# Performance work log

Hardware: AMD Instinct MI355X
Metric: run time of the kernel (lower is better)

## Reference

```python
import jax, jax.numpy as jnp
import numpy as np

SEQ_LEN = 4096
N_FEAT = 2048
N_PADD = 128


def setup_inputs() -> dict:
    key = jax.random.key(0)
    kx, kw = jax.random.split(key)
    x = jax.random.normal(kx, (SEQ_LEN, N_FEAT), dtype=jnp.float32)
    # Fused QKV dense: features = 3 * n_feat
    W = jax.random.normal(kw, (N_FEAT, 3 * N_FEAT), dtype=jnp.float32) * (1.0 / np.sqrt(N_FEAT))
    b = jnp.zeros((3 * N_FEAT,), dtype=jnp.float32)
    return {"x": x, "W": W, "b": b, "n_padd": N_PADD}


def reference(x, W, b, n_padd):
    # Fused QKV projection, split along feature axis (as in nn.Dense + jnp.split)
    qkv = x @ W + b  # [S, 3F]
    q, k, v = jnp.split(qkv, 3, axis=1)  # each [S, F]
    S, F = q.shape
    idx = jnp.arange(S)
    # scores[i, j] = q_i . k_j / sqrt(F)
    scores = (q @ k.T) * (1.0 / jnp.sqrt(jnp.float32(F)))  # [S, S]
    seq_mask = idx >= n_padd                      # valid (non-padding) positions
    causal = idx[None, :] <= idx[:, None]         # j <= i
    mask = causal & seq_mask[None, :]             # kernel: causal_mask & seq_mask
    row_valid = seq_mask                          # rows < n_padd are not computed/stored
    neg_inf = jnp.float32(-jnp.inf)
    scores = jnp.where(mask, scores, neg_inf)
    # Fully-masked (padding) rows would softmax to NaN; neutralize then zero output.
    scores = jnp.where(row_valid[:, None], scores, 0.0)
    att = jax.nn.softmax(scores, axis=-1)         # row-wise stable softmax
    out = att @ v                                 # [S, F]
    out = jnp.where(row_valid[:, None], out, 0.0)  # padded rows produce zeros
    return out
```

## Files before the change

### kernel.cpp

```cpp
#include <hip/hip_runtime.h>
#include <cstdint>
#include <cstddef>
#include <cmath>

typedef unsigned short u16;
typedef short v8s __attribute__((ext_vector_type(8)));
typedef float v4f __attribute__((ext_vector_type(4)));

constexpr int SEQ = 4096;
constexpr int FEAT = 2048;
constexpr int F3 = 6144;


__device__ __forceinline__ u16 f2bf(float f) {
  union { float f; uint32_t u; } v; v.f = f;
  uint32_t r = v.u + 0x7FFFu + ((v.u >> 16) & 1u);
  return (u16)(r >> 16);
}

__device__ __forceinline__ float bf2f(u16 s) {
  union { uint32_t u; float f; } v; v.u = ((uint32_t)s) << 16;
  return v.f;
}

__device__ __forceinline__ void gld_lds16(const u16* g, u16* l) {
  __builtin_amdgcn_global_load_lds(
      (const __attribute__((address_space(1))) void*)g,
      (__attribute__((address_space(3))) void*)l, 16, 0, 0);
}


__global__ void cvt_f32_bf16(const float* __restrict__ in, u16* __restrict__ out, int n8) {
  int i = blockIdx.x * 256 + threadIdx.x;
  if (i >= n8) return;
  const float4* p = (const float4*)in + (size_t)i * 2;
  float4 a = p[0], b = p[1];
  union { u16 s[8]; uint4 v; } u;
  u.s[0] = f2bf(a.x); u.s[1] = f2bf(a.y); u.s[2] = f2bf(a.z); u.s[3] = f2bf(a.w);
  u.s[4] = f2bf(b.x); u.s[5] = f2bf(b.y); u.s[6] = f2bf(b.z); u.s[7] = f2bf(b.w);
  *(uint4*)(out + (size_t)i * 8) = u.v;
}

__global__ void transp_f2b(const float* __restrict__ in, int ldin,
                           u16* __restrict__ out, int ldout) {
  __shared__ float tile[32][33];
  int c0 = blockIdx.x * 32, r0 = blockIdx.y * 32;
  int tx = threadIdx.x, ty = threadIdx.y;
#pragma unroll
  for (int p = 0; p < 4; ++p)
    tile[ty + 8 * p][tx] = in[(size_t)(r0 + ty + 8 * p) * ldin + c0 + tx];
  __syncthreads();
#pragma unroll
  for (int p = 0; p < 4; ++p)
    out[(size_t)(c0 + ty + 8 * p) * ldout + r0 + tx] = f2bf(tile[tx][ty + 8 * p]);
}

__global__ void transp_b2b(const u16* __restrict__ in, int ldin,
                           u16* __restrict__ out, int ldout) {
  __shared__ u16 tile[32][33];
  int c0 = blockIdx.x * 32, r0 = blockIdx.y * 32;
  int tx = threadIdx.x, ty = threadIdx.y;
#pragma unroll
  for (int p = 0; p < 4; ++p)
    tile[ty + 8 * p][tx] = in[(size_t)(r0 + ty + 8 * p) * ldin + c0 + tx];
  __syncthreads();
#pragma unroll
  for (int p = 0; p < 4; ++p)
    out[(size_t)(c0 + ty + 8 * p) * ldout + r0 + tx] = tile[tx][ty + 8 * p];
}


#define BARW()  asm volatile("s_barrier" ::: "memory")
#define VMC4() asm volatile("s_waitcnt vmcnt(4)" ::: "memory")

#define STAGE(SB, KO) do { \
  gld_lds16(Ag + (KO), &As[SB][0] + w * 512); \
  gld_lds16(Ag + (size_t)64 * LDA_ + (KO), &As[SB][0] + w * 512 + 2048); \
  gld_lds16(Bg + (KO), &Bs[SB][0] + w * 512); \
  gld_lds16(Bg + (size_t)64 * LDB_ + (KO), &Bs[SB][0] + w * 512 + 2048); \
} while (0)

#define LOADA(BUF) do { _Pragma("unroll") \
  for (int mi = 0; mi < 4; ++mi) \
    af[mi] = *(const v8s*)(&As[BUF][0] + (wr * 64 + mi * 16 + lm) * 32 + lqs); \
} while (0)

#define LOADB(BUF) do { _Pragma("unroll") \
  for (int ni = 0; ni < 4; ++ni) \
    bf4[ni] = *(const v8s*)(&Bs[BUF][0] + (wc * 64 + ni * 16 + lm) * 32 + lqs); \
} while (0)

template<int LDA_, int LDB_, int LDC_, int OUTMODE ,
         int ADDB, int CAUSAL, int SWZ>
__global__ __launch_bounds__(256, 3) void gemmw(
    const u16* __restrict__ A, const u16* __restrict__ B,
    void* __restrict__ Cv, int K,
    const float* __restrict__ bias, float scale) {
  int bi, bj, ks, ke;
  if (CAUSAL == 2) {
    const int b = blockIdx.x;
    const int cpx = gridDim.x >> 3;
    const int s = (b & 7) * cpx + (b >> 3);
    bi = (int)((sqrtf(8.f * s + 1.f) - 1.f) * 0.5f);
    while ((bi + 1) * (bi + 2) / 2 <= s) ++bi;
    while (bi * (bi + 1) / 2 > s) --bi;
    bj = s - bi * (bi + 1) / 2;
    ks = 0; ke = K;
  } else if (CAUSAL == 1) {
    bi = blockIdx.y; bj = blockIdx.x;
    if (blockIdx.z) bi = (int)gridDim.y - 1 - bi;
    const int kq = (bi + 1) * 64;
    ks = blockIdx.z ? kq : 0;  ke = ks + kq;
  } else {
    if (SWZ) {
      const int gx = gridDim.x, gy = gridDim.y;
      const int b = blockIdx.y * gx + blockIdx.x;
      const int cpx = (gx * gy) >> 3;
      const int s = (b & 7) * cpx + (b >> 3);
      bi = s % gy;  bj = s / gy;
    } else { bj = blockIdx.x; bi = blockIdx.y; }
    ks = 0; ke = K;
  }
  const int i0 = bi * 128, j0 = bj * 128;

  __shared__ u16 As[3][4096];
  __shared__ u16 Bs[3][4096];

  const int t = threadIdx.x;
  const int w = t >> 6, l = t & 63;
  const int wr = w >> 1, wc = w & 1;
  const int lm = l & 15, lq = l >> 4;
  const int lqs = ((lq + (lm >> 1)) & 3) * 8;

  const int srow = t >> 2;
  const int scol = (((t & 3) - ((t >> 3) & 3)) & 3) * 8;
  const u16* Ag = A + (size_t)(i0 + srow) * LDA_ + scol;
  const u16* Bg = B + (size_t)(j0 + srow) * LDB_ + scol;

  v4f acc[4][4];
#pragma unroll
  for (int a = 0; a < 4; ++a)
#pragma unroll
    for (int b2 = 0; b2 < 4; ++b2)
      acc[a][b2] = v4f{0.f, 0.f, 0.f, 0.f};

  v8s af[4], bf4[4];

  STAGE(0, ks); STAGE(1, ks + 32);
  VMC4(); BARW();
  LOADB(0);

  const int nt = (ke - ks) >> 5;
  int bufr = 0;
  int k2 = ks + 64;
  for (int tt = 0; tt < nt; ++tt) {
    const int sb = (bufr + 2 >= 3) ? bufr - 1 : bufr + 2;
    const int kst = (k2 < ke) ? k2 : ks;
    STAGE(sb, kst);
    LOADA(bufr);
    __builtin_amdgcn_s_setprio(1);
#pragma unroll
    for (int mi = 0; mi < 4; ++mi)
#pragma unroll
      for (int ni = 0; ni < 4; ++ni)
        acc[mi][ni] = __builtin_amdgcn_mfma_f32_16x16x32_bf16(af[mi], bf4[ni], acc[mi][ni], 0, 0, 0);
    __builtin_amdgcn_s_setprio(0);
    VMC4(); BARW();
    const int nb = (bufr == 2) ? 0 : bufr + 1;
    LOADB(nb);
    bufr = nb;
    k2 += 32;
  }

#pragma unroll
  for (int mi = 0; mi < 4; ++mi) {
#pragma unroll
    for (int ni = 0; ni < 4; ++ni) {
      const int cc = j0 + wc * 64 + ni * 16 + lm;
      const float badd = ADDB ? bias[cc] : 0.f;
#pragma unroll
      for (int r = 0; r < 4; ++r) {
        const int rr = i0 + wr * 64 + mi * 16 + lq * 4 + r;
        if (OUTMODE == 0)
          ((u16*)Cv)[(size_t)rr * LDC_ + cc] = f2bf(acc[mi][ni][r] * scale + badd);
        else
          atomicAdd((float*)Cv + (size_t)rr * LDC_ + cc, acc[mi][ni][r]);
      }
    }
  }
}

__global__ __launch_bounds__(256) void softmax_rows(
    const u16* __restrict__ S0,
    u16* __restrict__ att, const int* __restrict__ npad_p) {
  const int i = blockIdx.x;
  const int np = *npad_p;
  const int kend = ((i >> 7) + 1) << 7;
  const u16* r0 = S0 + (size_t)i * SEQ;
  u16* arow = att + (size_t)i * SEQ;
  const int t = threadIdx.x;

  float m = -3.0e38f, s = 0.f;
  for (int j = np + t; j <= i; j += 256) {
    float v = bf2f(r0[j]);
    if (v > m) { s = s * __expf(m - v) + 1.f; m = v; }
    else       { s += __expf(v - m); }
  }
#pragma unroll
  for (int off = 32; off > 0; off >>= 1) {
    float mo = __shfl_xor(m, off);
    float so = __shfl_xor(s, off);
    float M = fmaxf(m, mo);
    s = s * __expf(m - M) + so * __expf(mo - M);
    m = M;
  }
  __shared__ float sm[4], ss[4];
  const int w = t >> 6, l = t & 63;
  if (l == 0) { sm[w] = m; ss[w] = s; }
  __syncthreads();
  const float M = fmaxf(fmaxf(sm[0], sm[1]), fmaxf(sm[2], sm[3]));
  const float Ssum = ss[0] * __expf(sm[0] - M) + ss[1] * __expf(sm[1] - M) +
                     ss[2] * __expf(sm[2] - M) + ss[3] * __expf(sm[3] - M);
  const float inv = 1.f / Ssum;

  for (int j0b = t * 8; j0b < kend; j0b += 2048) {
    union { u16 s8[8]; uint4 v; } u;
#pragma unroll
    for (int q = 0; q < 8; ++q) {
      const int j = j0b + q;
      float a = 0.f;
      if (j >= np && j <= i)
        a = __expf(bf2f(r0[j]) - M) * inv;
      u.s8[q] = f2bf(a);
    }
    *(uint4*)(arow + j0b) = u.v;
  }
}


extern "C" void kernel_launch(void* const* d_in, const int* in_sizes, int n_in,
                              void* d_out, int out_size, void* d_ws, size_t ws_size,
                              hipStream_t stream) {
  const float* x = (const float*)d_in[0];
  const float* W = (const float*)d_in[1];
  const float* b = (const float*)d_in[2];
  const int* npad = (const int*)d_in[3];
  float* out = (float*)d_out;

  char* p = (char*)d_ws;
  u16* xb = (u16*)p;
  u16* Wt = (u16*)(p + (size_t)SEQ * FEAT * 2);
  u16* att = (u16*)p;
  p += (size_t)SEQ * FEAT * 2 + (size_t)F3 * FEAT * 2;
  u16* qkvb = (u16*)p;  p += (size_t)SEQ * F3 * 2;
  u16* vt   = (u16*)p;  p += (size_t)FEAT * SEQ * 2;
  u16* sc0  = (u16*)p;  p += (size_t)SEQ * SEQ * 2;
  if (ws_size < (size_t)(p - (char*)d_ws)) return;

  const float scale = 0.02209708691207961f;

  hipMemsetAsync(d_out, 0, (size_t)SEQ * FEAT * sizeof(float), stream);

  cvt_f32_bf16<<<SEQ * FEAT / 8 / 256, 256, 0, stream>>>(x, xb, SEQ * FEAT / 8);
  transp_f2b<<<dim3(F3 / 32, FEAT / 32), dim3(32, 8), 0, stream>>>(W, F3, Wt, FEAT);
  gemmw<FEAT, FEAT, F3, 0, 1, 0, 1><<<dim3(F3 / 128, SEQ / 128), 256, 0, stream>>>(
      xb, Wt, (void*)qkvb, FEAT, b, 1.0f);
  transp_b2b<<<dim3(FEAT / 32, SEQ / 32), dim3(32, 8), 0, stream>>>(
      qkvb + 2 * FEAT, F3, vt, SEQ);
  gemmw<F3, F3, SEQ, 0, 0, 2, 0><<<dim3(32 * 33 / 2), 256, 0, stream>>>(
      qkvb, qkvb + FEAT, (void*)sc0, FEAT, nullptr, scale);
  softmax_rows<<<SEQ, 256, 0, stream>>>(sc0, att, npad);
  gemmw<SEQ, SEQ, FEAT, 1, 0, 1, 0><<<dim3(FEAT / 128, SEQ / 128, 2), 256, 0, stream>>>(
      att, vt, (void*)out, 0, nullptr, 1.0f);
}
```

Before: 401.9 us.

## Widen GEMM tiles to 128x256 with unified LDS and remapped causal grids

Changes the shared GEMM kernel from 128x128 to 128x256 output tiles: each wave now computes all 128 rows against its own 64 columns, holding 8x4 accumulators. A and B are staged in one unified LDS buffer. The causal QK^T triangular index mapping is rewritten for 128x256 tiles, and the PV kernel's grid is linearized with row blocks ordered from longest K range to shortest. The goal is more reuse per loaded A fragment and fewer blocks. The cost is more registers and LDS per block, which lowers occupancy to 2 blocks per CU, and tiles on the causal diagonal do more wasted work.

After: 396.7 us. About the same (-1.3%).

```diff
diff --git a/kernel.cpp b/kernel.cpp
--- a/kernel.cpp
+++ b/kernel.cpp
@@ -70,47 +70,57 @@
 }
 
 
-#define BARW()  asm volatile("s_barrier" ::: "memory")
-#define VMC4() asm volatile("s_waitcnt vmcnt(4)" ::: "memory")
+#define BARW() asm volatile("s_barrier" ::: "memory")
+#define VMC6() asm volatile("s_waitcnt vmcnt(6)" ::: "memory")
 
 #define STAGE(SB, KO) do { \
-  gld_lds16(Ag + (KO), &As[SB][0] + w * 512); \
-  gld_lds16(Ag + (size_t)64 * LDA_ + (KO), &As[SB][0] + w * 512 + 2048); \
-  gld_lds16(Bg + (KO), &Bs[SB][0] + w * 512); \
-  gld_lds16(Bg + (size_t)64 * LDB_ + (KO), &Bs[SB][0] + w * 512 + 2048); \
+  u16* Lb = &LDSU[SB][0] + w * 512; \
+  gld_lds16(pA0 + (KO), Lb); \
+  gld_lds16(pA0 + (size_t)64 * LDA_ + (KO), Lb + 2048); \
+  gld_lds16(pB0 + (KO), Lb + 4096); \
+  gld_lds16(pB0 + (size_t)64 * LDB_ + (KO), Lb + 4096 + 2048); \
+  gld_lds16(pB0 + (size_t)128 * LDB_ + (KO), Lb + 4096 + 4096); \
+  gld_lds16(pB0 + (size_t)192 * LDB_ + (KO), Lb + 4096 + 6144); \
 } while (0)
 
 #define LOADA(BUF) do { _Pragma("unroll") \
-  for (int mi = 0; mi < 4; ++mi) \
-    af[mi] = *(const v8s*)(&As[BUF][0] + (wr * 64 + mi * 16 + lm) * 32 + lqs); \
+  for (int mi = 0; mi < 8; ++mi) \
+    af[mi] = *(const v8s*)(&LDSU[BUF][0] + (mi * 16 + lm) * 32 + lqs); \
 } while (0)
 
 #define LOADB(BUF) do { _Pragma("unroll") \
   for (int ni = 0; ni < 4; ++ni) \
-    bf4[ni] = *(const v8s*)(&Bs[BUF][0] + (wc * 64 + ni * 16 + lm) * 32 + lqs); \
+    bf4[ni] = *(const v8s*)(&LDSU[BUF][0] + 4096 + (w * 64 + ni * 16 + lm) * 32 + lqs); \
 } while (0)
 
+__device__ __forceinline__ int tri_S(int v) {
+  const int u = v >> 1;
+  return (v & 1) ? (u + 1) * (u + 1) : u * u + u;
+}
+
 template<int LDA_, int LDB_, int LDC_, int OUTMODE ,
-         int ADDB, int CAUSAL, int SWZ>
-__global__ __launch_bounds__(256, 3) void gemmw(
+         int ADDB, int MODE, int SWZ>
+__global__ __launch_bounds__(256, 2) void gemmw(
     const u16* __restrict__ A, const u16* __restrict__ B,
     void* __restrict__ Cv, int K,
     const float* __restrict__ bias, float scale) {
   int bi, bj, ks, ke;
-  if (CAUSAL == 2) {
+  if (MODE == 2) {
     const int b = blockIdx.x;
-    const int cpx = gridDim.x >> 3;
+    const int cpx = (int)gridDim.x >> 3;
     const int s = (b & 7) * cpx + (b >> 3);
-    bi = (int)((sqrtf(8.f * s + 1.f) - 1.f) * 0.5f);
-    while ((bi + 1) * (bi + 2) / 2 <= s) ++bi;
-    while (bi * (bi + 1) / 2 > s) --bi;
-    bj = s - bi * (bi + 1) / 2;
+    bi = 2 * (int)sqrtf((float)s);
+    while (tri_S(bi + 1) <= s) ++bi;
+    while (tri_S(bi) > s) --bi;
+    bj = s - tri_S(bi);
     ks = 0; ke = K;
-  } else if (CAUSAL == 1) {
-    bi = blockIdx.y; bj = blockIdx.x;
-    if (blockIdx.z) bi = (int)gridDim.y - 1 - bi;
+  } else if (MODE == 1) {
+    const int f = blockIdx.x;
+    bi = ((int)gridDim.x >> 4) - 1 - (f >> 4);
+    bj = (f >> 1) & 7;
+    const int z = f & 1;
     const int kq = (bi + 1) * 64;
-    ks = blockIdx.z ? kq : 0;  ke = ks + kq;
+    ks = z ? kq : 0;  ke = ks + kq;
   } else {
     if (SWZ) {
       const int gx = gridDim.x, gy = gridDim.y;
@@ -121,33 +131,32 @@
     } else { bj = blockIdx.x; bi = blockIdx.y; }
     ks = 0; ke = K;
   }
-  const int i0 = bi * 128, j0 = bj * 128;
-
-  __shared__ u16 As[3][4096];
-  __shared__ u16 Bs[3][4096];
+  const int i0 = bi * 128, j0 = bj * 256;
+
+  __shared__ u16 LDSU[3][12288];
 
   const int t = threadIdx.x;
   const int w = t >> 6, l = t & 63;
-  const int wr = w >> 1, wc = w & 1;
   const int lm = l & 15, lq = l >> 4;
   const int lqs = ((lq + (lm >> 1)) & 3) * 8;
 
-  const int srow = t >> 2;
-  const int scol = (((t & 3) - ((t >> 3) & 3)) & 3) * 8;
-  const u16* Ag = A + (size_t)(i0 + srow) * LDA_ + scol;
-  const u16* Bg = B + (size_t)(j0 + srow) * LDB_ + scol;
-
-  v4f acc[4][4];
-#pragma unroll
-  for (int a = 0; a < 4; ++a)
+  const int l2 = l >> 2;
+  const int rA = w * 16 + l2;
+  const int cA = ((((l & 3) - ((rA >> 1) & 3)) & 3)) * 8;
+  const u16* pA0 = A + (size_t)(i0 + rA) * LDA_ + cA;
+  const u16* pB0 = B + (size_t)(j0 + rA) * LDB_ + cA;
+
+  v4f acc[8][4];
+#pragma unroll
+  for (int a = 0; a < 8; ++a)
 #pragma unroll
     for (int b2 = 0; b2 < 4; ++b2)
       acc[a][b2] = v4f{0.f, 0.f, 0.f, 0.f};
 
-  v8s af[4], bf4[4];
+  v8s af[8], bf4[4];
 
   STAGE(0, ks); STAGE(1, ks + 32);
-  VMC4(); BARW();
+  VMC6(); BARW();
   LOADB(0);
 
   const int nt = (ke - ks) >> 5;
@@ -160,12 +169,12 @@
     LOADA(bufr);
     __builtin_amdgcn_s_setprio(1);
 #pragma unroll
-    for (int mi = 0; mi < 4; ++mi)
+    for (int mi = 0; mi < 8; ++mi)
 #pragma unroll
       for (int ni = 0; ni < 4; ++ni)
         acc[mi][ni] = __builtin_amdgcn_mfma_f32_16x16x32_bf16(af[mi], bf4[ni], acc[mi][ni], 0, 0, 0);
     __builtin_amdgcn_s_setprio(0);
-    VMC4(); BARW();
+    VMC6(); BARW();
     const int nb = (bufr == 2) ? 0 : bufr + 1;
     LOADB(nb);
     bufr = nb;
@@ -173,14 +182,14 @@
   }
 
 #pragma unroll
-  for (int mi = 0; mi < 4; ++mi) {
+  for (int mi = 0; mi < 8; ++mi) {
 #pragma unroll
     for (int ni = 0; ni < 4; ++ni) {
-      const int cc = j0 + wc * 64 + ni * 16 + lm;
+      const int cc = j0 + w * 64 + ni * 16 + lm;
       const float badd = ADDB ? bias[cc] : 0.f;
 #pragma unroll
       for (int r = 0; r < 4; ++r) {
-        const int rr = i0 + wr * 64 + mi * 16 + lq * 4 + r;
+        const int rr = i0 + mi * 16 + lq * 4 + r;
         if (OUTMODE == 0)
           ((u16*)Cv)[(size_t)rr * LDC_ + cc] = f2bf(acc[mi][ni][r] * scale + badd);
         else
@@ -263,13 +272,13 @@
 
   cvt_f32_bf16<<<SEQ * FEAT / 8 / 256, 256, 0, stream>>>(x, xb, SEQ * FEAT / 8);
   transp_f2b<<<dim3(F3 / 32, FEAT / 32), dim3(32, 8), 0, stream>>>(W, F3, Wt, FEAT);
-  gemmw<FEAT, FEAT, F3, 0, 1, 0, 1><<<dim3(F3 / 128, SEQ / 128), 256, 0, stream>>>(
+  gemmw<FEAT, FEAT, F3, 0, 1, 0, 1><<<dim3(F3 / 256, SEQ / 128), 256, 0, stream>>>(
       xb, Wt, (void*)qkvb, FEAT, b, 1.0f);
   transp_b2b<<<dim3(FEAT / 32, SEQ / 32), dim3(32, 8), 0, stream>>>(
       qkvb + 2 * FEAT, F3, vt, SEQ);
-  gemmw<F3, F3, SEQ, 0, 0, 2, 0><<<dim3(32 * 33 / 2), 256, 0, stream>>>(
+  gemmw<F3, F3, SEQ, 0, 0, 2, 0><<<dim3(272), 256, 0, stream>>>(
       qkvb, qkvb + FEAT, (void*)sc0, FEAT, nullptr, scale);
   softmax_rows<<<SEQ, 256, 0, stream>>>(sc0, att, npad);
-  gemmw<SEQ, SEQ, FEAT, 1, 0, 1, 0><<<dim3(FEAT / 128, SEQ / 128, 2), 256, 0, stream>>>(
+  gemmw<SEQ, SEQ, FEAT, 1, 0, 1, 0><<<dim3(512), 256, 0, stream>>>(
       att, vt, (void*)out, 0, nullptr, 1.0f);
 }
```
